# Optimization experiments

Hardware: AMD Instinct MI355X
Metric: run time of the kernel (lower is better)

Reference implementation:

```python
import jax, jax.numpy as jnp
import numpy as np

H = 1024      # hidden_size
NH = 16       # num_attention_heads
HD = H // NH  # head_size
DF = 4096     # ff intermediate
EPS = 1e-5


def layer_norm(x, g, b):
    mu = jnp.mean(x, axis=-1, keepdims=True)
    var = jnp.var(x, axis=-1, keepdims=True)
    return (x - mu) * jax.lax.rsqrt(var + EPS) * g + b


def setup_inputs() -> dict:
    key = jax.random.key(0)
    ks = jax.random.split(key, 4)
    s = 0.02
    return {
        "x": jax.random.normal(ks[0], (2, 2048, H), dtype=jnp.float32),
        "w_qkv": jax.random.normal(ks[1], (H, 3 * H), dtype=jnp.float32) * s,
        "ln1_g": jnp.ones((H,), jnp.float32),
        "ln1_b": jnp.zeros((H,), jnp.float32),
        "w1": jax.random.normal(ks[2], (H, DF), dtype=jnp.float32) * s,
        "b1": jnp.zeros((DF,), jnp.float32),
        "w2": jax.random.normal(ks[3], (DF, H), dtype=jnp.float32) * s,
        "b2": jnp.zeros((H,), jnp.float32),
        "ln2_g": jnp.ones((H,), jnp.float32),
        "ln2_b": jnp.zeros((H,), jnp.float32),
    }


def reference(x, w_qkv, ln1_g, ln1_b, w1, b1, w2, b2, ln2_g, ln2_b):
    b, s, h = x.shape
    # --- MHSelfAttention (naive) ---
    qkv = x @ w_qkv                                   # [b, s, 3h]
    qkv = qkv.reshape(b, s, 3, NH, HD)
    q, k, v = (jnp.moveaxis(qkv, 2, 0)                # [3, b, s, nh, hd]
               .transpose(0, 1, 3, 2, 4))             # [3, b, nh, s, hd]
    # NOTE: faithful quirk — scaled by sqrt(hidden_size), not head_size
    scores = jnp.einsum('bnqd,bnkd->bnqk', q, k) / jnp.sqrt(jnp.float32(h))
    probs = jax.nn.softmax(scores, axis=-1)
    ctx = jnp.einsum('bnqk,bnkd->bnqd', probs, v)     # [b, nh, s, hd]
    attn_out = ctx.transpose(0, 2, 1, 3).reshape(b, s, h)
    # post-norm residual (dropout = identity in eval)
    x = x + layer_norm(attn_out, ln1_g, ln1_b)
    # --- FFN ---
    ff = jax.nn.relu(x @ w1 + b1) @ w2 + b2
    x = x + layer_norm(ff, ln2_g, ln2_b)
    return x
```

## Files before the change

kernel.cpp:

```cpp
#include <hip/hip_runtime.h>


typedef unsigned short u16;
typedef unsigned int u32;
typedef __bf16 bf16x8 __attribute__((ext_vector_type(8)));
typedef float f32x4 __attribute__((ext_vector_type(4)));
typedef u32 u32x4 __attribute__((ext_vector_type(4)));
typedef u16 u16x4 __attribute__((ext_vector_type(4)));

__device__ __forceinline__ u16 f2b(float f) {
  u32 u = __builtin_bit_cast(u32, f);
  u += 0x7fffu + ((u >> 16) & 1u);
  return (u16)(u >> 16);
}
__device__ __forceinline__ float b2f(u16 u) {
  return __builtin_bit_cast(float, (u32)u << 16);
}

__device__ __forceinline__ void gld_lds16(const u16* g, u16* l) {
  __builtin_amdgcn_global_load_lds(
      (const __attribute__((address_space(1))) u32*)g,
      (__attribute__((address_space(3))) u32*)l, 16, 0, 0);
}

__global__ __launch_bounds__(256) void convert_bf16_kernel(
    const float* __restrict__ in, u16* __restrict__ out) {
  const int idx = blockIdx.x * 256 + threadIdx.x;
  float4 v = ((const float4*)in)[idx];
  u16x4 o = { f2b(v.x), f2b(v.y), f2b(v.z), f2b(v.w) };
  ((u16x4*)out)[idx] = o;
}

__global__ __launch_bounds__(256) void transpose_bf16_kernel(
    const float* __restrict__ in, u16* __restrict__ out, int R, int C) {
  __shared__ float tile[32][33];
  const int cb = blockIdx.x * 32, rb = blockIdx.y * 32;
  const int c = threadIdx.x & 31;
  const int r0 = threadIdx.x >> 5;
#pragma unroll
  for (int rr = 0; rr < 32; rr += 8)
    tile[r0 + rr][c] = in[(size_t)(rb + r0 + rr) * C + cb + c];
  __syncthreads();
#pragma unroll
  for (int rr = 0; rr < 32; rr += 8)
    out[(size_t)(cb + r0 + rr) * R + rb + c] = f2b(tile[c][r0 + rr]);
}

__global__ __launch_bounds__(256) void transpose_v_kernel(
    const u16* __restrict__ qkv, u16* __restrict__ vt) {
  __shared__ u16 t[64][70];
  const int bh = blockIdx.x, st = blockIdx.y;
  const int b = bh >> 4, nh = bh & 15;
  const int s0 = st * 64;
  const int r = threadIdx.x >> 3, c = (threadIdx.x & 7) << 3;
  const u16* src = qkv + (size_t)(b * 2048 + s0) * 3072 + 2048 + nh * 64;
#pragma unroll
  for (int rr = 0; rr < 64; rr += 32)
    *(u32x4*)&t[r + rr][c] = *(const u32x4*)(src + (size_t)(r + rr) * 3072 + c);
  __syncthreads();
  u16* dst = vt + ((size_t)bh * 64) * 2048 + s0;
#pragma unroll
  for (int rr = 0; rr < 64; rr += 32) {
    const int d = r + rr;
    u16 tmp[8];
#pragma unroll
    for (int j = 0; j < 8; ++j) tmp[j] = t[c + j][d];
    *(u32x4*)(dst + (size_t)d * 2048 + c) = *(u32x4*)tmp;
  }
}

__global__ __launch_bounds__(256) void gemm_bt_kernel(
    const u16* __restrict__ A, const u16* __restrict__ Bt,
    const float* __restrict__ bias, float* __restrict__ Cf, u16* __restrict__ Cb,
    int M, int N, int K, int relu,
    u16* __restrict__ Cb1, u16* __restrict__ Cb2, u16* __restrict__ Cb3) {
  const int bid = blockIdx.x;
  const int xcd = bid & 7;
  const int g = bid >> 3;
  const int m0 = (xcd * 4 + (g & 3)) * 128;
  const int n0 = (g >> 2) * 128;
  const int z = blockIdx.y;
  const int kn = K / (int)gridDim.y;
  if (z == 1) Cb = Cb1; else if (z == 2) Cb = Cb2; else if (z == 3) Cb = Cb3;
  const int tid = threadIdx.x;
  const int w = tid >> 6, lane = tid & 63, quad = lane >> 4, l16 = lane & 15;
  const int wm = (w & 1) * 64, wn = (w >> 1) * 64;

  __shared__ u16 As[2][128][32];
  __shared__ u16 Bs[2][128][32];

  f32x4 acc[4][4];
#pragma unroll
  for (int i = 0; i < 4; ++i)
#pragma unroll
    for (int j = 0; j < 4; ++j) acc[i][j] = {0.f, 0.f, 0.f, 0.f};

  const int srow = w * 16 + (lane >> 2);
  const int scol = (lane & 3) << 3;
  const u16* Ag = A + (size_t)(m0 + srow) * K + scol + (size_t)z * kn;
  const u16* Bg = Bt + (size_t)(n0 + srow) * K + scol + (size_t)z * kn;
  const size_t rstep = (size_t)64 * K;

  for (int k0 = 0; k0 < kn; k0 += 64) {
    __syncthreads();
    gld_lds16(Ag + k0,              &As[0][w * 16][0]);
    gld_lds16(Ag + k0 + 32,         &As[1][w * 16][0]);
    gld_lds16(Ag + rstep + k0,      &As[0][64 + w * 16][0]);
    gld_lds16(Ag + rstep + k0 + 32, &As[1][64 + w * 16][0]);
    gld_lds16(Bg + k0,              &Bs[0][w * 16][0]);
    gld_lds16(Bg + k0 + 32,         &Bs[1][w * 16][0]);
    gld_lds16(Bg + rstep + k0,      &Bs[0][64 + w * 16][0]);
    gld_lds16(Bg + rstep + k0 + 32, &Bs[1][64 + w * 16][0]);
    __syncthreads();

#pragma unroll
    for (int s = 0; s < 2; ++s) {
      bf16x8 af[4], bfr[4];
#pragma unroll
      for (int i = 0; i < 4; ++i)
        af[i] = *(const bf16x8*)&As[s][wm + i * 16 + l16][quad * 8];
#pragma unroll
      for (int j = 0; j < 4; ++j)
        bfr[j] = *(const bf16x8*)&Bs[s][wn + j * 16 + l16][quad * 8];
#pragma unroll
      for (int i = 0; i < 4; ++i)
#pragma unroll
        for (int j = 0; j < 4; ++j)
          acc[i][j] = __builtin_amdgcn_mfma_f32_16x16x32_bf16(af[i], bfr[j], acc[i][j], 0, 0, 0);
    }
  }

#pragma unroll
  for (int i = 0; i < 4; ++i) {
    const int row = m0 + wm + i * 16 + quad * 4;
#pragma unroll
    for (int j = 0; j < 4; ++j) {
      const int col = n0 + wn + j * 16 + l16;
      const float bv = bias ? bias[col] : 0.f;
#pragma unroll
      for (int r = 0; r < 4; ++r) {
        float v = acc[i][j][r] + bv;
        if (relu) v = fmaxf(v, 0.f);
        const size_t idx = (size_t)(row + r) * N + col;
        if (Cf) Cf[idx] = v;
        if (Cb) Cb[idx] = f2b(v);
      }
    }
  }
}

__global__ __launch_bounds__(256, 4) void attn_kernel(
    const u16* __restrict__ qkv, const u16* __restrict__ vt,
    float* __restrict__ Op0, float* __restrict__ Op1,
    float* __restrict__ lpart) {
  const int bh = blockIdx.x;
  const int qt = blockIdx.y;
  const int kz = blockIdx.z;
  const int b = bh >> 4, nh = bh & 15;
  const int tid = threadIdx.x;
  const int w = tid >> 6, lane = tid & 63, quad = lane >> 4, l16 = lane & 15;
  const float c2 = 0.04508422f;

  __shared__ u16 KH[2][64][32];
  __shared__ u16 VH[2][64][32];
  __shared__ u16 QP[4][32][68];

  u16 (*Qs)[68] = (u16(*)[68])&QP[0][0][0];

  const size_t rs = 3072;
  const u16* qbase = qkv + (size_t)b * 2048 * rs + nh * 64;
  const u16* kbase = qbase + 1024;
  const u16* vbase = vt + (size_t)bh * 64 * 2048;
  const int q0 = qt * 128;
  const int k0beg = kz * 1024;

  {
    const int row = tid >> 1, colb = (tid & 1) << 5;
#pragma unroll
    for (int h = 0; h < 4; ++h) {
      u32x4 v = *(const u32x4*)(qbase + (size_t)(q0 + row) * rs + colb + h * 8);
      u16 ti[8], to[8];
      *(u32x4*)ti = v;
#pragma unroll
      for (int j = 0; j < 8; ++j) to[j] = f2b(b2f(ti[j]) * c2);
      *(u32x4*)&Qs[row][colb + h * 8] = *(u32x4*)to;
    }
  }
  __syncthreads();

  bf16x8 aq[2][2];
#pragma unroll
  for (int mi = 0; mi < 2; ++mi)
#pragma unroll
    for (int d0 = 0; d0 < 2; ++d0)
      aq[mi][d0] = *(const bf16x8*)&Qs[w * 32 + mi * 16 + l16][d0 * 32 + quad * 8];

  bf16x8 ones;
#pragma unroll
  for (int j = 0; j < 8; ++j) ones[j] = (__bf16)1.0f;

  f32x4 Oacc[2][4], l_acc[2];
#pragma unroll
  for (int mi = 0; mi < 2; ++mi) {
    l_acc[mi] = {0.f, 0.f, 0.f, 0.f};
#pragma unroll
    for (int jt = 0; jt < 4; ++jt) Oacc[mi][jt] = {0.f, 0.f, 0.f, 0.f};
  }

  const int drow = lane >> 2;
  const int dcol = (lane & 3) << 3;

#pragma unroll 1
  for (int t = 0; t < 16; ++t) {
    const int k0 = k0beg + t * 64;
    __syncthreads();
    gld_lds16(kbase + (size_t)(k0 + w * 16 + drow) * rs + dcol,        &KH[0][w * 16][0]);
    gld_lds16(kbase + (size_t)(k0 + w * 16 + drow) * rs + 32 + dcol,   &KH[1][w * 16][0]);
    gld_lds16(vbase + (size_t)(w * 16 + drow) * 2048 + k0 + dcol,      &VH[0][w * 16][0]);
    gld_lds16(vbase + (size_t)(w * 16 + drow) * 2048 + k0 + 32 + dcol, &VH[1][w * 16][0]);
    __syncthreads();

    f32x4 S[2][4];
#pragma unroll
    for (int mi = 0; mi < 2; ++mi)
#pragma unroll
      for (int jt = 0; jt < 4; ++jt) S[mi][jt] = {0.f, 0.f, 0.f, 0.f};
#pragma unroll
    for (int d0 = 0; d0 < 2; ++d0)
#pragma unroll
      for (int jt = 0; jt < 4; ++jt) {
        bf16x8 bv = *(const bf16x8*)&KH[d0][jt * 16 + l16][quad * 8];
        S[0][jt] = __builtin_amdgcn_mfma_f32_16x16x32_bf16(aq[0][d0], bv, S[0][jt], 0, 0, 0);
        S[1][jt] = __builtin_amdgcn_mfma_f32_16x16x32_bf16(aq[1][d0], bv, S[1][jt], 0, 0, 0);
      }

#pragma unroll
    for (int mi = 0; mi < 2; ++mi)
#pragma unroll
      for (int jt = 0; jt < 4; ++jt)
#pragma unroll
        for (int r = 0; r < 4; ++r) {
          float p = exp2f(S[mi][jt][r]);
          QP[w][mi * 16 + quad * 4 + r][jt * 16 + l16] =
              (u16)(__builtin_bit_cast(u32, p) >> 16);
        }

    bf16x8 ap[2][2];
#pragma unroll
    for (int mi = 0; mi < 2; ++mi)
#pragma unroll
      for (int kk = 0; kk < 2; ++kk)
        ap[mi][kk] = *(const bf16x8*)&QP[w][mi * 16 + l16][kk * 32 + quad * 8];
#pragma unroll
    for (int kk = 0; kk < 2; ++kk) {
#pragma unroll
      for (int jt = 0; jt < 4; ++jt) {
        bf16x8 bv = *(const bf16x8*)&VH[kk][jt * 16 + l16][quad * 8];
        Oacc[0][jt] = __builtin_amdgcn_mfma_f32_16x16x32_bf16(ap[0][kk], bv, Oacc[0][jt], 0, 0, 0);
        Oacc[1][jt] = __builtin_amdgcn_mfma_f32_16x16x32_bf16(ap[1][kk], bv, Oacc[1][jt], 0, 0, 0);
      }
      l_acc[0] = __builtin_amdgcn_mfma_f32_16x16x32_bf16(ap[0][kk], ones, l_acc[0], 0, 0, 0);
      l_acc[1] = __builtin_amdgcn_mfma_f32_16x16x32_bf16(ap[1][kk], ones, l_acc[1], 0, 0, 0);
    }
  }

  float* opart = kz ? Op1 : Op0;
  float* obase = opart + (size_t)b * 2048 * 1024 + (size_t)nh * 64;
  float* lbase = lpart + (size_t)kz * 4096 * 16 + (size_t)b * 2048 * 16 + nh;
#pragma unroll
  for (int mi = 0; mi < 2; ++mi) {
    const int qrow = q0 + w * 32 + mi * 16 + quad * 4;
#pragma unroll
    for (int r = 0; r < 4; ++r) {
#pragma unroll
      for (int jt = 0; jt < 4; ++jt)
        obase[(size_t)(qrow + r) * 1024 + jt * 16 + l16] = Oacc[mi][jt][r];
      if (l16 == 0) lbase[(size_t)(qrow + r) * 16] = l_acc[mi][r];
    }
  }
}

__global__ __launch_bounds__(256) void ln_attn_kernel(
    const float* __restrict__ O0, const float* __restrict__ O1,
    const float* __restrict__ l0, const float* __restrict__ l1,
    const float* __restrict__ xres, const float* __restrict__ g,
    const float* __restrict__ bb, float* __restrict__ outf,
    u16* __restrict__ outb) {
  const int row = blockIdx.x;
  const int tid = threadIdx.x;
  const int w = tid >> 6, lane = tid & 63;
  const int head = tid >> 4;
  float4 a0 = ((const float4*)(O0 + (size_t)row * 1024))[tid];
  float4 a1 = ((const float4*)(O1 + (size_t)row * 1024))[tid];
  const float inv = 1.f / (l0[row * 16 + head] + l1[row * 16 + head]);
  float4 v;
  v.x = (a0.x + a1.x) * inv;
  v.y = (a0.y + a1.y) * inv;
  v.z = (a0.z + a1.z) * inv;
  v.w = (a0.w + a1.w) * inv;
  float s = v.x + v.y + v.z + v.w;
  float s2 = v.x * v.x + v.y * v.y + v.z * v.z + v.w * v.w;
#pragma unroll
  for (int off = 32; off > 0; off >>= 1) {
    s += __shfl_xor(s, off);
    s2 += __shfl_xor(s2, off);
  }
  __shared__ float red[8];
  if (lane == 0) { red[w] = s; red[4 + w] = s2; }
  __syncthreads();
  s = red[0] + red[1] + red[2] + red[3];
  s2 = red[4] + red[5] + red[6] + red[7];
  const float mu = s * (1.f / 1024.f);
  const float var = s2 * (1.f / 1024.f) - mu * mu;
  const float rstd = rsqrtf(var + 1e-5f);
  float4 xr = ((const float4*)(xres + (size_t)row * 1024))[tid];
  float4 gv = ((const float4*)g)[tid];
  float4 bv = ((const float4*)bb)[tid];
  float4 o;
  o.x = xr.x + (v.x - mu) * rstd * gv.x + bv.x;
  o.y = xr.y + (v.y - mu) * rstd * gv.y + bv.y;
  o.z = xr.z + (v.z - mu) * rstd * gv.z + bv.z;
  o.w = xr.w + (v.w - mu) * rstd * gv.w + bv.w;
  ((float4*)(outf + (size_t)row * 1024))[tid] = o;
  u16x4 ob = { f2b(o.x), f2b(o.y), f2b(o.z), f2b(o.w) };
  *(u16x4*)(outb + (size_t)row * 1024 + (size_t)tid * 4) = ob;
}

__global__ __launch_bounds__(256) void ln_ffn_kernel(
    const u16* __restrict__ p0, const u16* __restrict__ p1,
    const u16* __restrict__ p2, const u16* __restrict__ p3,
    const float* __restrict__ bias, const float* __restrict__ xres,
    const float* __restrict__ g, const float* __restrict__ bb,
    float* __restrict__ outf) {
  const int row = blockIdx.x;
  const int tid = threadIdx.x;
  const int w = tid >> 6, lane = tid & 63;
  u16x4 a0 = ((const u16x4*)(p0 + (size_t)row * 1024))[tid];
  u16x4 a1 = ((const u16x4*)(p1 + (size_t)row * 1024))[tid];
  u16x4 a2 = ((const u16x4*)(p2 + (size_t)row * 1024))[tid];
  u16x4 a3 = ((const u16x4*)(p3 + (size_t)row * 1024))[tid];
  float4 bv4 = ((const float4*)bias)[tid];
  float4 v;
  v.x = (b2f(a0[0]) + b2f(a1[0])) + (b2f(a2[0]) + b2f(a3[0])) + bv4.x;
  v.y = (b2f(a0[1]) + b2f(a1[1])) + (b2f(a2[1]) + b2f(a3[1])) + bv4.y;
  v.z = (b2f(a0[2]) + b2f(a1[2])) + (b2f(a2[2]) + b2f(a3[2])) + bv4.z;
  v.w = (b2f(a0[3]) + b2f(a1[3])) + (b2f(a2[3]) + b2f(a3[3])) + bv4.w;
  float s = v.x + v.y + v.z + v.w;
  float s2 = v.x * v.x + v.y * v.y + v.z * v.z + v.w * v.w;
#pragma unroll
  for (int off = 32; off > 0; off >>= 1) {
    s += __shfl_xor(s, off);
    s2 += __shfl_xor(s2, off);
  }
  __shared__ float red[8];
  if (lane == 0) { red[w] = s; red[4 + w] = s2; }
  __syncthreads();
  s = red[0] + red[1] + red[2] + red[3];
  s2 = red[4] + red[5] + red[6] + red[7];
  const float mu = s * (1.f / 1024.f);
  const float var = s2 * (1.f / 1024.f) - mu * mu;
  const float rstd = rsqrtf(var + 1e-5f);
  float4 xr = ((const float4*)(xres + (size_t)row * 1024))[tid];
  float4 gv = ((const float4*)g)[tid];
  float4 bv = ((const float4*)bb)[tid];
  float4 o;
  o.x = xr.x + (v.x - mu) * rstd * gv.x + bv.x;
  o.y = xr.y + (v.y - mu) * rstd * gv.y + bv.y;
  o.z = xr.z + (v.z - mu) * rstd * gv.z + bv.z;
  o.w = xr.w + (v.w - mu) * rstd * gv.w + bv.w;
  ((float4*)(outf + (size_t)row * 1024))[tid] = o;
}

extern "C" void kernel_launch(void* const* d_in, const int* in_sizes, int n_in,
                              void* d_out, int out_size, void* d_ws, size_t ws_size,
                              hipStream_t stream) {
  const float* x     = (const float*)d_in[0];
  const float* w_qkv = (const float*)d_in[1];
  const float* ln1_g = (const float*)d_in[2];
  const float* ln1_b = (const float*)d_in[3];
  const float* w1    = (const float*)d_in[4];
  const float* b1    = (const float*)d_in[5];
  const float* w2    = (const float*)d_in[6];
  const float* b2    = (const float*)d_in[7];
  const float* ln2_g = (const float*)d_in[8];
  const float* ln2_b = (const float*)d_in[9];
  float* out = (float*)d_out;
  char* ws = (char*)d_ws;

  u16*   xb    = (u16*)(ws + 0);
  u16*   wqkvT = (u16*)(ws + 8388608);
  u16*   qkvb  = (u16*)(ws + 31457280);
  u16*   vT    = (u16*)(ws + 56623104);
  float* Op0   = (float*)(ws + 0);
  float* Op1   = (float*)(ws + 73400320);
  float* lp    = (float*)(ws + 90177536);
  float* x1    = (float*)(ws + 31457280);
  u16*   x1b   = (u16*)(ws + 48234496);
  u16*   w1T   = (u16*)(ws + 14680064);
  u16*   w2T   = (u16*)(ws + 23068672);
  u16*   h1    = (u16*)(ws + 56623104);
  u16*   fp0   = (u16*)(ws + 0);
  u16*   fp1   = (u16*)(ws + 8388608);
  u16*   fp2   = (u16*)(ws + 48234496);
  u16*   fp3   = (u16*)(ws + 90177536);

  convert_bf16_kernel<<<4096, 256, 0, stream>>>(x, xb);
  transpose_bf16_kernel<<<dim3(96, 32), 256, 0, stream>>>(w_qkv, wqkvT, 1024, 3072);

  gemm_bt_kernel<<<dim3(32 * 24, 1), 256, 0, stream>>>(
      xb, wqkvT, nullptr, nullptr, qkvb, 4096, 3072, 1024, 0,
      nullptr, nullptr, nullptr);
  transpose_v_kernel<<<dim3(32, 32), 256, 0, stream>>>(qkvb, vT);
  attn_kernel<<<dim3(32, 16, 2), 256, 0, stream>>>(qkvb, vT, Op0, Op1, lp);

  ln_attn_kernel<<<4096, 256, 0, stream>>>(
      Op0, Op1, lp, lp + 4096 * 16, x, ln1_g, ln1_b, x1, x1b);

  transpose_bf16_kernel<<<dim3(128, 32), 256, 0, stream>>>(w1, w1T, 1024, 4096);
  transpose_bf16_kernel<<<dim3(32, 128), 256, 0, stream>>>(w2, w2T, 4096, 1024);

  gemm_bt_kernel<<<dim3(32 * 32, 1), 256, 0, stream>>>(
      x1b, w1T, b1, nullptr, h1, 4096, 4096, 1024, 1,
      nullptr, nullptr, nullptr);
  gemm_bt_kernel<<<dim3(32 * 8, 4), 256, 0, stream>>>(
      h1, w2T, nullptr, nullptr, fp0, 4096, 1024, 4096, 0,
      fp1, fp2, fp3);

  ln_ffn_kernel<<<4096, 256, 0, stream>>>(
      fp0, fp1, fp2, fp3, b2, x1, ln2_g, ln2_b, out);
}
```

Before: 349.3 us.

## Fuse V transpose into QKV GEMM, fold Q scale into weights, bf16 attention partials

The QKV GEMM epilogue now writes the V columns straight into the transposed V layout, which removes the separate transpose_v kernel. The softmax scale is folded into the Q columns of the transposed QKV weight, so the attention kernel loads Q directly into LDS with global_load_lds instead of scaling it element by element. The attention partial outputs are stored as bf16 instead of fp32, which halves the traffic into the layernorm kernel. Costs: the V stores in the GEMM epilogue are strided 8-byte writes, and the extra bf16 rounding of Q, the weights and the partial outputs may lower accuracy.

```diff
diff --git a/kernel.cpp b/kernel.cpp
--- a/kernel.cpp
+++ b/kernel.cpp
@@ -32,7 +32,8 @@
 }
 
 __global__ __launch_bounds__(256) void transpose_bf16_kernel(
-    const float* __restrict__ in, u16* __restrict__ out, int R, int C) {
+    const float* __restrict__ in, u16* __restrict__ out, int R, int C,
+    int scale_cols, float scale) {
   __shared__ float tile[32][33];
   const int cb = blockIdx.x * 32, rb = blockIdx.y * 32;
   const int c = threadIdx.x & 31;
@@ -42,30 +43,10 @@
     tile[r0 + rr][c] = in[(size_t)(rb + r0 + rr) * C + cb + c];
   __syncthreads();
 #pragma unroll
-  for (int rr = 0; rr < 32; rr += 8)
-    out[(size_t)(cb + r0 + rr) * R + rb + c] = f2b(tile[c][r0 + rr]);
-}
-
-__global__ __launch_bounds__(256) void transpose_v_kernel(
-    const u16* __restrict__ qkv, u16* __restrict__ vt) {
-  __shared__ u16 t[64][70];
-  const int bh = blockIdx.x, st = blockIdx.y;
-  const int b = bh >> 4, nh = bh & 15;
-  const int s0 = st * 64;
-  const int r = threadIdx.x >> 3, c = (threadIdx.x & 7) << 3;
-  const u16* src = qkv + (size_t)(b * 2048 + s0) * 3072 + 2048 + nh * 64;
-#pragma unroll
-  for (int rr = 0; rr < 64; rr += 32)
-    *(u32x4*)&t[r + rr][c] = *(const u32x4*)(src + (size_t)(r + rr) * 3072 + c);
-  __syncthreads();
-  u16* dst = vt + ((size_t)bh * 64) * 2048 + s0;
-#pragma unroll
-  for (int rr = 0; rr < 64; rr += 32) {
-    const int d = r + rr;
-    u16 tmp[8];
-#pragma unroll
-    for (int j = 0; j < 8; ++j) tmp[j] = t[c + j][d];
-    *(u32x4*)(dst + (size_t)d * 2048 + c) = *(u32x4*)tmp;
+  for (int rr = 0; rr < 32; rr += 8) {
+    const int n = cb + r0 + rr;
+    const float sc = (n < scale_cols) ? scale : 1.f;
+    out[(size_t)n * R + rb + c] = f2b(tile[c][r0 + rr] * sc);
   }
 }
 
@@ -73,7 +54,8 @@
     const u16* __restrict__ A, const u16* __restrict__ Bt,
     const float* __restrict__ bias, float* __restrict__ Cf, u16* __restrict__ Cb,
     int M, int N, int K, int relu,
-    u16* __restrict__ Cb1, u16* __restrict__ Cb2, u16* __restrict__ Cb3) {
+    u16* __restrict__ Cb1, u16* __restrict__ Cb2, u16* __restrict__ Cb3,
+    u16* __restrict__ Vt) {
   const int bid = blockIdx.x;
   const int xcd = bid & 7;
   const int g = bid >> 3;
@@ -130,6 +112,23 @@
     }
   }
 
+  if (Vt && n0 >= 2048) {
+#pragma unroll
+    for (int i = 0; i < 4; ++i) {
+      const int row = m0 + wm + i * 16 + quad * 4;
+      const int b_ = row >> 11, s = row & 2047;
+#pragma unroll
+      for (int j = 0; j < 4; ++j) {
+        const int vcol = n0 + wn + j * 16 + l16 - 2048;
+        u16* dst = Vt + ((size_t)((b_ << 4) + (vcol >> 6)) * 64 + (vcol & 63)) * 2048 + s;
+        u16x4 o = { f2b(acc[i][j][0]), f2b(acc[i][j][1]),
+                    f2b(acc[i][j][2]), f2b(acc[i][j][3]) };
+        *(u16x4*)dst = o;
+      }
+    }
+    return;
+  }
+
 #pragma unroll
   for (int i = 0; i < 4; ++i) {
     const int row = m0 + wm + i * 16 + quad * 4;
@@ -151,7 +150,7 @@
 
 __global__ __launch_bounds__(256, 4) void attn_kernel(
     const u16* __restrict__ qkv, const u16* __restrict__ vt,
-    float* __restrict__ Op0, float* __restrict__ Op1,
+    u16* __restrict__ Op0, u16* __restrict__ Op1,
     float* __restrict__ lpart) {
   const int bh = blockIdx.x;
   const int qt = blockIdx.y;
@@ -159,13 +158,11 @@
   const int b = bh >> 4, nh = bh & 15;
   const int tid = threadIdx.x;
   const int w = tid >> 6, lane = tid & 63, quad = lane >> 4, l16 = lane & 15;
-  const float c2 = 0.04508422f;
 
   __shared__ u16 KH[2][64][32];
   __shared__ u16 VH[2][64][32];
   __shared__ u16 QP[4][32][68];
-
-  u16 (*Qs)[68] = (u16(*)[68])&QP[0][0][0];
+  u16 (*Qs)[128][32] = (u16 (*)[128][32])&QP[0][0][0];
 
   const size_t rs = 3072;
   const u16* qbase = qkv + (size_t)b * 2048 * rs + nh * 64;
@@ -174,18 +171,15 @@
   const int q0 = qt * 128;
   const int k0beg = kz * 1024;
 
-  {
-    const int row = tid >> 1, colb = (tid & 1) << 5;
-#pragma unroll
-    for (int h = 0; h < 4; ++h) {
-      u32x4 v = *(const u32x4*)(qbase + (size_t)(q0 + row) * rs + colb + h * 8);
-      u16 ti[8], to[8];
-      *(u32x4*)ti = v;
-#pragma unroll
-      for (int j = 0; j < 8; ++j) to[j] = f2b(b2f(ti[j]) * c2);
-      *(u32x4*)&Qs[row][colb + h * 8] = *(u32x4*)to;
-    }
-  }
+  const int drow = lane >> 2;
+  const int dcol = (lane & 3) << 3;
+
+#pragma unroll
+  for (int rr = 0; rr < 128; rr += 64)
+#pragma unroll
+    for (int h = 0; h < 2; ++h)
+      gld_lds16(qbase + (size_t)(q0 + rr + w * 16 + drow) * rs + h * 32 + dcol,
+                &Qs[h][rr + w * 16][0]);
   __syncthreads();
 
   bf16x8 aq[2][2];
@@ -193,7 +187,7 @@
   for (int mi = 0; mi < 2; ++mi)
 #pragma unroll
     for (int d0 = 0; d0 < 2; ++d0)
-      aq[mi][d0] = *(const bf16x8*)&Qs[w * 32 + mi * 16 + l16][d0 * 32 + quad * 8];
+      aq[mi][d0] = *(const bf16x8*)&Qs[d0][w * 32 + mi * 16 + l16][quad * 8];
 
   bf16x8 ones;
 #pragma unroll
@@ -206,9 +200,6 @@
 #pragma unroll
     for (int jt = 0; jt < 4; ++jt) Oacc[mi][jt] = {0.f, 0.f, 0.f, 0.f};
   }
-
-  const int drow = lane >> 2;
-  const int dcol = (lane & 3) << 3;
 
 #pragma unroll 1
   for (int t = 0; t < 16; ++t) {
@@ -264,8 +255,8 @@
     }
   }
 
-  float* opart = kz ? Op1 : Op0;
-  float* obase = opart + (size_t)b * 2048 * 1024 + (size_t)nh * 64;
+  u16* opart = kz ? Op1 : Op0;
+  u16* obase = opart + (size_t)b * 2048 * 1024 + (size_t)nh * 64;
   float* lbase = lpart + (size_t)kz * 4096 * 16 + (size_t)b * 2048 * 16 + nh;
 #pragma unroll
   for (int mi = 0; mi < 2; ++mi) {
@@ -274,14 +265,14 @@
     for (int r = 0; r < 4; ++r) {
 #pragma unroll
       for (int jt = 0; jt < 4; ++jt)
-        obase[(size_t)(qrow + r) * 1024 + jt * 16 + l16] = Oacc[mi][jt][r];
+        obase[(size_t)(qrow + r) * 1024 + jt * 16 + l16] = f2b(Oacc[mi][jt][r]);
       if (l16 == 0) lbase[(size_t)(qrow + r) * 16] = l_acc[mi][r];
     }
   }
 }
 
 __global__ __launch_bounds__(256) void ln_attn_kernel(
-    const float* __restrict__ O0, const float* __restrict__ O1,
+    const u16* __restrict__ O0, const u16* __restrict__ O1,
     const float* __restrict__ l0, const float* __restrict__ l1,
     const float* __restrict__ xres, const float* __restrict__ g,
     const float* __restrict__ bb, float* __restrict__ outf,
@@ -290,14 +281,14 @@
   const int tid = threadIdx.x;
   const int w = tid >> 6, lane = tid & 63;
   const int head = tid >> 4;
-  float4 a0 = ((const float4*)(O0 + (size_t)row * 1024))[tid];
-  float4 a1 = ((const float4*)(O1 + (size_t)row * 1024))[tid];
+  u16x4 a0 = ((const u16x4*)(O0 + (size_t)row * 1024))[tid];
+  u16x4 a1 = ((const u16x4*)(O1 + (size_t)row * 1024))[tid];
   const float inv = 1.f / (l0[row * 16 + head] + l1[row * 16 + head]);
   float4 v;
-  v.x = (a0.x + a1.x) * inv;
-  v.y = (a0.y + a1.y) * inv;
-  v.z = (a0.z + a1.z) * inv;
-  v.w = (a0.w + a1.w) * inv;
+  v.x = (b2f(a0[0]) + b2f(a1[0])) * inv;
+  v.y = (b2f(a0[1]) + b2f(a1[1])) * inv;
+  v.z = (b2f(a0[2]) + b2f(a1[2])) * inv;
+  v.w = (b2f(a0[3]) + b2f(a1[3])) * inv;
   float s = v.x + v.y + v.z + v.w;
   float s2 = v.x * v.x + v.y * v.y + v.z * v.z + v.w * v.w;
 #pragma unroll
@@ -387,12 +378,14 @@
   float* out = (float*)d_out;
   char* ws = (char*)d_ws;
 
+  const float c2 = 0.04508422f;
+
   u16*   xb    = (u16*)(ws + 0);
   u16*   wqkvT = (u16*)(ws + 8388608);
   u16*   qkvb  = (u16*)(ws + 31457280);
   u16*   vT    = (u16*)(ws + 56623104);
-  float* Op0   = (float*)(ws + 0);
-  float* Op1   = (float*)(ws + 73400320);
+  u16*   Op0   = (u16*)(ws + 0);
+  u16*   Op1   = (u16*)(ws + 73400320);
   float* lp    = (float*)(ws + 90177536);
   float* x1    = (float*)(ws + 31457280);
   u16*   x1b   = (u16*)(ws + 48234496);
@@ -405,26 +398,26 @@
   u16*   fp3   = (u16*)(ws + 90177536);
 
   convert_bf16_kernel<<<4096, 256, 0, stream>>>(x, xb);
-  transpose_bf16_kernel<<<dim3(96, 32), 256, 0, stream>>>(w_qkv, wqkvT, 1024, 3072);
+  transpose_bf16_kernel<<<dim3(96, 32), 256, 0, stream>>>(w_qkv, wqkvT, 1024, 3072,
+                                                          1024, c2);
 
   gemm_bt_kernel<<<dim3(32 * 24, 1), 256, 0, stream>>>(
       xb, wqkvT, nullptr, nullptr, qkvb, 4096, 3072, 1024, 0,
-      nullptr, nullptr, nullptr);
-  transpose_v_kernel<<<dim3(32, 32), 256, 0, stream>>>(qkvb, vT);
+      nullptr, nullptr, nullptr, vT);
   attn_kernel<<<dim3(32, 16, 2), 256, 0, stream>>>(qkvb, vT, Op0, Op1, lp);
 
   ln_attn_kernel<<<4096, 256, 0, stream>>>(
       Op0, Op1, lp, lp + 4096 * 16, x, ln1_g, ln1_b, x1, x1b);
 
-  transpose_bf16_kernel<<<dim3(128, 32), 256, 0, stream>>>(w1, w1T, 1024, 4096);
-  transpose_bf16_kernel<<<dim3(32, 128), 256, 0, stream>>>(w2, w2T, 4096, 1024);
+  transpose_bf16_kernel<<<dim3(128, 32), 256, 0, stream>>>(w1, w1T, 1024, 4096, 0, 1.f);
+  transpose_bf16_kernel<<<dim3(32, 128), 256, 0, stream>>>(w2, w2T, 4096, 1024, 0, 1.f);
 
   gemm_bt_kernel<<<dim3(32 * 32, 1), 256, 0, stream>>>(
       x1b, w1T, b1, nullptr, h1, 4096, 4096, 1024, 1,
-      nullptr, nullptr, nullptr);
+      nullptr, nullptr, nullptr, nullptr);
   gemm_bt_kernel<<<dim3(32 * 8, 4), 256, 0, stream>>>(
       h1, w2T, nullptr, nullptr, fp0, 4096, 1024, 4096, 0,
-      fp1, fp2, fp3);
+      fp1, fp2, fp3, nullptr);
 
   ln_ffn_kernel<<<4096, 256, 0, stream>>>(
       fp0, fp1, fp2, fp3, b2, x1, ln2_g, ln2_b, out);
```

Result: no change. 351.9 us (+0.7%).
